# Kernel optimization log

Hardware: AMD Instinct MI355X
Metric: run time of the kernel (lower is better)

## Reference

```python
import jax, jax.numpy as jnp
import numpy as np

Q, V = 16384, 4096  # query batch (captions), video batch


def setup_inputs() -> dict:
    key = jax.random.key(0)
    q2ctx_scores = jax.random.normal(key, (Q, V), dtype=jnp.float32)
    # each query labeled with a video; arange % V guarantees every video has >=1 query
    labels = jnp.arange(Q, dtype=jnp.int64) % V
    return {"q2ctx_scores": q2ctx_scores, "labels": labels}


def reference(q2ctx_scores, labels):
    # q2ctx_scores: [Q, V], labels: [Q] int in [0, V)
    Qn, Vn = q2ctx_scores.shape
    # t2v: nominator is the matched score (logsumexp over a single element is identity)
    s = jnp.take_along_axis(q2ctx_scores, labels[:, None], axis=1)[:, 0]  # [Q]
    t2v_denominator = jax.nn.logsumexp(q2ctx_scores, axis=1)              # [Q]
    # v2t nominator: segmented logsumexp of matched scores grouped by video label
    m = jax.ops.segment_max(s, labels, num_segments=Vn)                   # [V]
    seg_sum = jax.ops.segment_sum(jnp.exp(s - m[labels]), labels, num_segments=Vn)
    v2t_nominator = m + jnp.log(seg_sum)                                  # [V]
    v2t_denominator = jax.nn.logsumexp(q2ctx_scores, axis=0)              # [V]
    return jnp.mean(t2v_denominator - s) + jnp.mean(v2t_denominator - v2t_nominator)
```

## Files before the change

kernel.cpp:

```cpp
#include <hip/hip_runtime.h>
#include <hip/hip_bf16.h>


#define QN 16384
#define VN 4096
#define NB 2048
#define TB 256
#define STEP (NB * TB)
#define ITERS ((QN * (VN / 4)) / STEP)
#define ROWS_PER_STEP (STEP / (VN / 4))

typedef float f32x4 __attribute__((ext_vector_type(4)));

#define COLCOMP_OFF 0
#define ROWSUM_OFF  (NB * 1024)
#define NOMSUM_OFF  (ROWSUM_OFF + QN)
#define COLSUM_OFF  (NOMSUM_OFF + VN)
#define ACC_OFF     (COLSUM_OFF + VN)

__global__ __launch_bounds__(256) void init_pass(float* __restrict__ ws) {
    int i = blockIdx.x * 256 + threadIdx.x;
    int n = QN + VN + VN + 8;
    if (i < n) ws[ROWSUM_OFF + i] = 0.0f;
}

__global__ __launch_bounds__(256) void gather_pass(const float* __restrict__ scores,
                                                   const int* __restrict__ labels,
                                                   float* __restrict__ ws) {
    float* nomsum = ws + NOMSUM_OFF;
    float* acc    = ws + ACC_OFF;
    const int i = blockIdx.x * 256 + threadIdx.x;
    const int lab = labels[i];
    const float s = scores[(size_t)i * VN + lab];
    unsafeAtomicAdd(&nomsum[lab], __expf(s));
    float v = s;
#pragma unroll
    for (int off = 32; off >= 1; off >>= 1)
        v += __shfl_down(v, off);
    if ((threadIdx.x & 63) == 0) unsafeAtomicAdd(&acc[1], v);
}

__global__ __launch_bounds__(256, 8) void main_pass(const float* __restrict__ scores,
                                                    float* __restrict__ ws) {
    float* rowsum  = ws + ROWSUM_OFF;
    float* colcomp = ws + COLCOMP_OFF;
    const int tid  = threadIdx.x;
    const int b    = blockIdx.x;
    const int lane = tid & 63;
    const f32x4* sp = reinterpret_cast<const f32x4*>(scores);
    const int base = b * TB + tid;
    const int rowInStep = base >> 10;

    float c0 = 0.f, c1 = 0.f, c2 = 0.f, c3 = 0.f;

#pragma unroll 8
    for (int k = 0; k < ITERS; ++k) {
        f32x4 x = __builtin_nontemporal_load(&sp[(size_t)k * STEP + base]);
        float e0 = __expf(x.x), e1 = __expf(x.y);
        float e2 = __expf(x.z), e3 = __expf(x.w);
        c0 += e0; c1 += e1; c2 += e2; c3 += e3;
        float rp = (e0 + e1) + (e2 + e3);
#pragma unroll
        for (int off = 32; off >= 1; off >>= 1)
            rp += __shfl_down(rp, off);
        if (lane == 0)
            unsafeAtomicAdd(&rowsum[k * ROWS_PER_STEP + rowInStep], rp);
    }

    f32x4 o; o.x = c0; o.y = c1; o.z = c2; o.w = c3;
    reinterpret_cast<f32x4*>(colcomp)[b * TB + tid] = o;
}

__global__ __launch_bounds__(256) void reduce_pass(float* __restrict__ ws) {
    const float* colcomp = ws + COLCOMP_OFF;
    const float* rowsum  = ws + ROWSUM_OFF;
    float* colsum = ws + COLSUM_OFF;
    float* acc    = ws + ACC_OFF;
    const int tid = threadIdx.x;

    if (blockIdx.x < 128) {
        const int q  = blockIdx.x >> 5;
        const int cc = (blockIdx.x >> 3) & 3;
        const int mg = blockIdx.x & 7;
        const int c  = cc * 256 + tid;
        float sum = 0.0f;
#pragma unroll 4
        for (int m = mg * 64; m < mg * 64 + 64; ++m)
            sum += colcomp[(size_t)(4 * m + q) * 1024 + c];
        unsafeAtomicAdd(&colsum[q * 1024 + c], sum);
    } else {
        const int idx = (blockIdx.x - 128) * 256 + tid;
        float v = __logf(rowsum[idx]);
#pragma unroll
        for (int off = 32; off >= 1; off >>= 1)
            v += __shfl_down(v, off);
        if ((tid & 63) == 0) unsafeAtomicAdd(&acc[0], v);
    }
}

__global__ __launch_bounds__(256) void final_pass(const float* __restrict__ ws,
                                                  float* __restrict__ out) {
    const float* nomsum = ws + NOMSUM_OFF;
    const float* colsum = ws + COLSUM_OFF;
    const float* acc    = ws + ACC_OFF;
    const int tid = threadIdx.x;

    float local = 0.0f;
    for (int c = tid; c < VN; c += 256)
        local += __logf(colsum[c]) - __logf(nomsum[c]);
#pragma unroll
    for (int off = 32; off >= 1; off >>= 1)
        local += __shfl_down(local, off);
    __shared__ float red[4];
    const int wid = tid >> 6, lane = tid & 63;
    if (lane == 0) red[wid] = local;
    __syncthreads();
    if (tid == 0) {
        const float v2t = (red[0] + red[1]) + (red[2] + red[3]);
        out[0] = (acc[0] - acc[1]) * (1.0f / QN) + v2t * (1.0f / VN);
    }
}

extern "C" void kernel_launch(void* const* d_in, const int* in_sizes, int n_in,
                              void* d_out, int out_size, void* d_ws, size_t ws_size,
                              hipStream_t stream) {
    const float* scores = (const float*)d_in[0];
    const int*   labels = (const int*)d_in[1];
    float* ws  = (float*)d_ws;
    float* out = (float*)d_out;

    init_pass<<<(QN + VN + VN + 8 + 255) / 256, 256, 0, stream>>>(ws);
    gather_pass<<<QN / 256, 256, 0, stream>>>(scores, labels, ws);
    main_pass<<<NB, TB, 0, stream>>>(scores, ws);
    reduce_pass<<<192, 256, 0, stream>>>(ws);
    final_pass<<<1, 256, 0, stream>>>(ws, out);
}
```

Baseline: 365.2 us.

## Fuse label gather into main pass and merge reduce/final via ticket

Folds the per-query matched-score gather into the streaming main pass, where the thread owning the labelled column picks it out of the values it has already loaded. Row partial sums are accumulated in shared memory and flushed once per block instead of one global atomic per wavefront per iteration. The reduce and final kernels are merged using a last-block ticket counter, and the init kernel is replaced by a memset. This cuts kernel launches and the scattered gather reads, at the cost of a per-iteration label load and branch inside the hot loop.

After: 404.0 us. 10.6% more time.

```diff
diff --git a/kernel.cpp b/kernel.cpp
--- a/kernel.cpp
+++ b/kernel.cpp
@@ -1,5 +1,4 @@
 #include <hip/hip_runtime.h>
-#include <hip/hip_bf16.h>
 
 
 #define QN 16384
@@ -17,45 +16,37 @@
 #define NOMSUM_OFF  (ROWSUM_OFF + QN)
 #define COLSUM_OFF  (NOMSUM_OFF + VN)
 #define ACC_OFF     (COLSUM_OFF + VN)
-
-__global__ __launch_bounds__(256) void init_pass(float* __restrict__ ws) {
-    int i = blockIdx.x * 256 + threadIdx.x;
-    int n = QN + VN + VN + 8;
-    if (i < n) ws[ROWSUM_OFF + i] = 0.0f;
-}
-
-__global__ __launch_bounds__(256) void gather_pass(const float* __restrict__ scores,
-                                                   const int* __restrict__ labels,
-                                                   float* __restrict__ ws) {
-    float* nomsum = ws + NOMSUM_OFF;
-    float* acc    = ws + ACC_OFF;
-    const int i = blockIdx.x * 256 + threadIdx.x;
-    const int lab = labels[i];
-    const float s = scores[(size_t)i * VN + lab];
-    unsafeAtomicAdd(&nomsum[lab], __expf(s));
-    float v = s;
-#pragma unroll
-    for (int off = 32; off >= 1; off >>= 1)
-        v += __shfl_down(v, off);
-    if ((threadIdx.x & 63) == 0) unsafeAtomicAdd(&acc[1], v);
-}
+#define TICKET_OFF  (ACC_OFF + 4)
+#define ZERO_FLOATS (QN + VN + VN + 8)
 
 __global__ __launch_bounds__(256, 8) void main_pass(const float* __restrict__ scores,
+                                                    const int* __restrict__ labels,
                                                     float* __restrict__ ws) {
     float* rowsum  = ws + ROWSUM_OFF;
+    float* nomsum  = ws + NOMSUM_OFF;
     float* colcomp = ws + COLCOMP_OFF;
+    float* acc     = ws + ACC_OFF;
     const int tid  = threadIdx.x;
     const int b    = blockIdx.x;
     const int lane = tid & 63;
     const f32x4* sp = reinterpret_cast<const f32x4*>(scores);
-    const int base = b * TB + tid;
-    const int rowInStep = base >> 10;
+    const int base      = b * TB + tid;
+    const int rowInStep = b >> 2;
+    const int quarter   = b & 3;
+
+    __shared__ float rowacc[ITERS];
+    if (tid < ITERS) rowacc[tid] = 0.0f;
+    __syncthreads();
 
     float c0 = 0.f, c1 = 0.f, c2 = 0.f, c3 = 0.f;
+    float sAcc = 0.f;
+    bool matched = false;
 
 #pragma unroll 8
     for (int k = 0; k < ITERS; ++k) {
         f32x4 x = __builtin_nontemporal_load(&sp[(size_t)k * STEP + base]);
+        const int row = k * ROWS_PER_STEP + rowInStep;
+        const int lab = labels[row];
         float e0 = __expf(x.x), e1 = __expf(x.y);
         float e2 = __expf(x.z), e3 = __expf(x.w);
         c0 += e0; c1 += e1; c2 += e2; c3 += e3;
@@ -63,19 +54,35 @@
 #pragma unroll
         for (int off = 32; off >= 1; off >>= 1)
             rp += __shfl_down(rp, off);
-        if (lane == 0)
-            unsafeAtomicAdd(&rowsum[k * ROWS_PER_STEP + rowInStep], rp);
+        if (lane == 0) atomicAdd(&rowacc[k], rp);
+        if ((lab >> 10) == quarter && ((lab >> 2) & 255) == tid) {
+            const int j = lab & 3;
+            const float sj = (j == 0) ? x.x : (j == 1) ? x.y : (j == 2) ? x.z : x.w;
+            const float ej = (j == 0) ? e0 : (j == 1) ? e1 : (j == 2) ? e2 : e3;
+            unsafeAtomicAdd(&nomsum[lab], ej);
+            sAcc += sj;
+            matched = true;
+        }
     }
 
     f32x4 o; o.x = c0; o.y = c1; o.z = c2; o.w = c3;
     reinterpret_cast<f32x4*>(colcomp)[b * TB + tid] = o;
+
+    __syncthreads();
+    if (tid < ITERS)
+        unsafeAtomicAdd(&rowsum[tid * ROWS_PER_STEP + rowInStep], rowacc[tid]);
+    if (matched)
+        unsafeAtomicAdd(&acc[1], sAcc);
 }
 
-__global__ __launch_bounds__(256) void reduce_pass(float* __restrict__ ws) {
+__global__ __launch_bounds__(256) void reduce_final(float* __restrict__ ws,
+                                                    float* __restrict__ out) {
     const float* colcomp = ws + COLCOMP_OFF;
     const float* rowsum  = ws + ROWSUM_OFF;
     float* colsum = ws + COLSUM_OFF;
+    float* nomsum = ws + NOMSUM_OFF;
     float* acc    = ws + ACC_OFF;
+    int* ticket   = reinterpret_cast<int*>(ws + TICKET_OFF);
     const int tid = threadIdx.x;
 
     if (blockIdx.x < 128) {
@@ -96,18 +103,19 @@
             v += __shfl_down(v, off);
         if ((tid & 63) == 0) unsafeAtomicAdd(&acc[0], v);
     }
-}
 
-__global__ __launch_bounds__(256) void final_pass(const float* __restrict__ ws,
-                                                  float* __restrict__ out) {
-    const float* nomsum = ws + NOMSUM_OFF;
-    const float* colsum = ws + COLSUM_OFF;
-    const float* acc    = ws + ACC_OFF;
-    const int tid = threadIdx.x;
+    __threadfence();
+    __shared__ int amLast;
+    if (tid == 0) amLast = (atomicAdd(ticket, 1) == 191);
+    __syncthreads();
+    if (!amLast) return;
 
     float local = 0.0f;
-    for (int c = tid; c < VN; c += 256)
-        local += __logf(colsum[c]) - __logf(nomsum[c]);
+    for (int c = tid; c < VN; c += 256) {
+        const float cs = atomicAdd(&colsum[c], 0.0f);
+        const float ns = atomicAdd(&nomsum[c], 0.0f);
+        local += __logf(cs) - __logf(ns);
+    }
 #pragma unroll
     for (int off = 32; off >= 1; off >>= 1)
         local += __shfl_down(local, off);
@@ -116,8 +124,10 @@
     if (lane == 0) red[wid] = local;
     __syncthreads();
     if (tid == 0) {
+        const float a0 = atomicAdd(&acc[0], 0.0f);
+        const float a1 = atomicAdd(&acc[1], 0.0f);
         const float v2t = (red[0] + red[1]) + (red[2] + red[3]);
-        out[0] = (acc[0] - acc[1]) * (1.0f / QN) + v2t * (1.0f / VN);
+        out[0] = (a0 - a1) * (1.0f / QN) + v2t * (1.0f / VN);
     }
 }
 
@@ -129,9 +139,7 @@
     float* ws  = (float*)d_ws;
     float* out = (float*)d_out;
 
-    init_pass<<<(QN + VN + VN + 8 + 255) / 256, 256, 0, stream>>>(ws);
-    gather_pass<<<QN / 256, 256, 0, stream>>>(scores, labels, ws);
-    main_pass<<<NB, TB, 0, stream>>>(scores, ws);
-    reduce_pass<<<192, 256, 0, stream>>>(ws);
-    final_pass<<<1, 256, 0, stream>>>(ws, out);
+    hipMemsetAsync(ws + ROWSUM_OFF, 0, ZERO_FLOATS * sizeof(float), stream);
+    main_pass<<<NB, TB, 0, stream>>>(scores, labels, ws);
+    reduce_final<<<192, 256, 0, stream>>>(ws, out);
 }
```

## Give each block a contiguous 8-row tile and reduce per-block column partials

Applied to the files above, without the earlier changes.

The main pass now assigns each block 8 contiguous rows (32 KB float4 chunks) instead of a grid-strided layout. Each thread keeps four sets of column accumulators, one per row phase, and writes a full 4096-wide partial. The reduce pass then sums 2048 such partials per column. The colcomp workspace grows fourfold, so the reduce pass reads more data in exchange for contiguous streaming loads. The init kernel is also replaced with hipMemsetAsync.

Result: no change. 372.2 us (+1.9%).

```diff
diff --git a/kernel.cpp b/kernel.cpp
--- a/kernel.cpp
+++ b/kernel.cpp
@@ -1,28 +1,21 @@
 #include <hip/hip_runtime.h>
-#include <hip/hip_bf16.h>
 
 
 #define QN 16384
 #define VN 4096
 #define NB 2048
 #define TB 256
-#define STEP (NB * TB)
-#define ITERS ((QN * (VN / 4)) / STEP)
-#define ROWS_PER_STEP (STEP / (VN / 4))
+#define ITERS 32
+#define F4_PER_BLOCK 8192
 
 typedef float f32x4 __attribute__((ext_vector_type(4)));
 
 #define COLCOMP_OFF 0
-#define ROWSUM_OFF  (NB * 1024)
+#define ROWSUM_OFF  (NB * 4096)
 #define NOMSUM_OFF  (ROWSUM_OFF + QN)
 #define COLSUM_OFF  (NOMSUM_OFF + VN)
 #define ACC_OFF     (COLSUM_OFF + VN)
-
-__global__ __launch_bounds__(256) void init_pass(float* __restrict__ ws) {
-    int i = blockIdx.x * 256 + threadIdx.x;
-    int n = QN + VN + VN + 8;
-    if (i < n) ws[ROWSUM_OFF + i] = 0.0f;
-}
+#define ZERO_FLOATS (QN + VN + VN + 8)
 
 __global__ __launch_bounds__(256) void gather_pass(const float* __restrict__ scores,
                                                    const int* __restrict__ labels,
@@ -48,27 +41,38 @@
     const int b    = blockIdx.x;
     const int lane = tid & 63;
     const f32x4* sp = reinterpret_cast<const f32x4*>(scores);
-    const int base = b * TB + tid;
-    const int rowInStep = base >> 10;
+    const size_t base = (size_t)b * F4_PER_BLOCK + tid;
 
-    float c0 = 0.f, c1 = 0.f, c2 = 0.f, c3 = 0.f;
+    float c00=0.f,c01=0.f,c02=0.f,c03=0.f;
+    float c10=0.f,c11=0.f,c12=0.f,c13=0.f;
+    float c20=0.f,c21=0.f,c22=0.f,c23=0.f;
+    float c30=0.f,c31=0.f,c32=0.f,c33=0.f;
 
 #pragma unroll 8
     for (int k = 0; k < ITERS; ++k) {
-        f32x4 x = __builtin_nontemporal_load(&sp[(size_t)k * STEP + base]);
+        f32x4 x = __builtin_nontemporal_load(&sp[base + k * 256]);
         float e0 = __expf(x.x), e1 = __expf(x.y);
         float e2 = __expf(x.z), e3 = __expf(x.w);
-        c0 += e0; c1 += e1; c2 += e2; c3 += e3;
+        switch (k & 3) {
+            case 0: c00 += e0; c01 += e1; c02 += e2; c03 += e3; break;
+            case 1: c10 += e0; c11 += e1; c12 += e2; c13 += e3; break;
+            case 2: c20 += e0; c21 += e1; c22 += e2; c23 += e3; break;
+            case 3: c30 += e0; c31 += e1; c32 += e2; c33 += e3; break;
+        }
         float rp = (e0 + e1) + (e2 + e3);
 #pragma unroll
         for (int off = 32; off >= 1; off >>= 1)
             rp += __shfl_down(rp, off);
         if (lane == 0)
-            unsafeAtomicAdd(&rowsum[k * ROWS_PER_STEP + rowInStep], rp);
+            unsafeAtomicAdd(&rowsum[b * 8 + (k >> 2)], rp);
     }
 
-    f32x4 o; o.x = c0; o.y = c1; o.z = c2; o.w = c3;
-    reinterpret_cast<f32x4*>(colcomp)[b * TB + tid] = o;
+    f32x4* cc = reinterpret_cast<f32x4*>(colcomp + (size_t)b * 4096);
+    f32x4 o;
+    o.x=c00; o.y=c01; o.z=c02; o.w=c03; cc[0 * 256 + tid] = o;
+    o.x=c10; o.y=c11; o.z=c12; o.w=c13; cc[1 * 256 + tid] = o;
+    o.x=c20; o.y=c21; o.z=c22; o.w=c23; cc[2 * 256 + tid] = o;
+    o.x=c30; o.y=c31; o.z=c32; o.w=c33; cc[3 * 256 + tid] = o;
 }
 
 __global__ __launch_bounds__(256) void reduce_pass(float* __restrict__ ws) {
@@ -79,15 +83,14 @@
     const int tid = threadIdx.x;
 
     if (blockIdx.x < 128) {
-        const int q  = blockIdx.x >> 5;
-        const int cc = (blockIdx.x >> 3) & 3;
-        const int mg = blockIdx.x & 7;
-        const int c  = cc * 256 + tid;
+        const int mg = blockIdx.x >> 4;
+        const int cb = blockIdx.x & 15;
+        const int c  = cb * 256 + tid;
         float sum = 0.0f;
 #pragma unroll 4
-        for (int m = mg * 64; m < mg * 64 + 64; ++m)
-            sum += colcomp[(size_t)(4 * m + q) * 1024 + c];
-        unsafeAtomicAdd(&colsum[q * 1024 + c], sum);
+        for (int m = mg * 256; m < mg * 256 + 256; ++m)
+            sum += colcomp[(size_t)m * 4096 + c];
+        unsafeAtomicAdd(&colsum[c], sum);
     } else {
         const int idx = (blockIdx.x - 128) * 256 + tid;
         float v = __logf(rowsum[idx]);
@@ -129,7 +132,7 @@
     float* ws  = (float*)d_ws;
     float* out = (float*)d_out;
 
-    init_pass<<<(QN + VN + VN + 8 + 255) / 256, 256, 0, stream>>>(ws);
+    hipMemsetAsync(ws + ROWSUM_OFF, 0, ZERO_FLOATS * sizeof(float), stream);
     gather_pass<<<QN / 256, 256, 0, stream>>>(scores, labels, ws);
     main_pass<<<NB, TB, 0, stream>>>(scores, ws);
     reduce_pass<<<192, 256, 0, stream>>>(ws);
```
